# Kernel optimization log

Hardware: AMD Instinct MI355X
Metric: run time of the kernel (lower is better)

## Reference

```python
import jax, jax.numpy as jnp
import numpy as np


def _layer_norm(x, w, b, eps=1e-5):
    mu = jnp.mean(x, axis=-1, keepdims=True)
    var = jnp.mean((x - mu) ** 2, axis=-1, keepdims=True)
    return (x - mu) / jnp.sqrt(var + eps) * w + b


def _s4_block(u, log_dt, A_re, A_im, C_re, C_im, D, out_w, out_b):
    # u: (B, L, H). S4D diagonal SSM, bidirectional, ZOH discretization.
    B, L, H = u.shape
    dt = jnp.exp(log_dt)                       # (H,)
    A = A_re + 1j * A_im                       # (H, N) complex64
    dtA = A * dt[:, None]                      # (H, N)
    C = C_re + 1j * C_im                       # (2, H, N)
    Ct = C * ((jnp.exp(dtA) - 1.0) / A)        # (2, H, N)  ZOH input matrix folded into C
    vand = jnp.exp(dtA[:, :, None] * jnp.arange(L))   # (H, N, L) vandermonde of exp(dt*A)
    K = 2.0 * jnp.einsum('chn,hnl->chl', Ct, vand).real  # (2, H, L); 2*Re for conj pairs
    # bidirectional kernel laid out over length 2L (forward causal + flipped anticausal)
    k = jnp.pad(K[0], ((0, 0), (0, L))) + jnp.pad(jnp.flip(K[1], -1), ((0, 0), (L, 0)))
    k_f = jnp.fft.rfft(k, n=2 * L, axis=-1)    # (H, L+1)
    u_f = jnp.fft.rfft(u, n=2 * L, axis=1)     # (B, L+1, H)
    y = jnp.fft.irfft(u_f * k_f.T[None], n=2 * L, axis=1)[:, :L]  # (B, L, H)
    y = y + u * D                              # skip connection D*u
    y = jax.nn.gelu(y, approximate=False)      # torch GELU is exact erf form
    z = y @ out_w.T + out_b                    # (B, L, 2H) output linear
    return z[..., :H] * jax.nn.sigmoid(z[..., H:])  # GLU


def setup_inputs() -> dict:
    key = jax.random.key(0)
    ks = jax.random.split(key, 10)
    B, L, H, N, NL = 8, 4096, 512, 16, 4
    x = jax.random.normal(ks[0], (B, 1, L), dtype=jnp.float32)
    enc_w = jax.random.normal(ks[1], (H, 2), dtype=jnp.float32) * 0.1
    enc_b = jnp.zeros((H,), jnp.float32)
    # S4D-Lin init: dt log-uniform in [1e-3, 1e-1], A = -0.5 + i*pi*n
    log_dt = np.log(1e-3) + jax.random.uniform(ks[2], (NL, H), dtype=jnp.float32) * (np.log(1e-1) - np.log(1e-3))
    A_re = -0.5 * jnp.ones((NL, H, N), jnp.float32)
    A_im = jnp.broadcast_to(np.pi * jnp.arange(N, dtype=jnp.float32), (NL, H, N))
    C_re = jax.random.normal(ks[3], (NL, 2, H, N), dtype=jnp.float32) * 0.5
    C_im = jax.random.normal(ks[4], (NL, 2, H, N), dtype=jnp.float32) * 0.5
    D = jax.random.normal(ks[5], (NL, H), dtype=jnp.float32)
    out_w = jax.random.normal(ks[6], (NL, 2 * H, H), dtype=jnp.float32) / np.sqrt(H)
    out_b = jnp.zeros((NL, 2 * H), jnp.float32)
    ln_w = jnp.ones((NL, H), jnp.float32)
    ln_b = jnp.zeros((NL, H), jnp.float32)
    dec_w = jax.random.normal(ks[7], (1, H), dtype=jnp.float32) / np.sqrt(H)
    dec_b = jnp.zeros((1,), jnp.float32)
    return dict(x=x, enc_w=enc_w, enc_b=enc_b, log_dt=log_dt, A_re=A_re, A_im=A_im,
                C_re=C_re, C_im=C_im, D=D, out_w=out_w, out_b=out_b,
                ln_w=ln_w, ln_b=ln_b, dec_w=dec_w, dec_b=dec_b)


def reference(x, enc_w, enc_b, log_dt, A_re, A_im, C_re, C_im, D, out_w, out_b, ln_w, ln_b, dec_w, dec_b):
    B, _, L = x.shape
    grid = jnp.linspace(0.0, 1.0, L, dtype=x.dtype)                    # get_grid with grid=None
    h = jnp.concatenate([x.transpose(0, 2, 1),
                         jnp.broadcast_to(grid[None, :, None], (B, L, 1))], axis=-1)  # (B, L, 2)
    h = h @ enc_w.T + enc_b                                            # encoder -> (B, L, H)
    n_layers = log_dt.shape[0]
    for i in range(n_layers):                                          # prenorm residual stack
        z = _layer_norm(h, ln_w[i], ln_b[i])
        z = _s4_block(z, log_dt[i], A_re[i], A_im[i], C_re[i], C_im[i], D[i], out_w[i], out_b[i])
        h = z + h                                                      # dropout is identity (eval)
    y = h @ dec_w.T + dec_b                                            # decoder -> (B, L, 1)
    return y.transpose(0, 2, 1)                                        # (B, 1, L)
```

## Files before the change

kernel.cpp:

```cpp
#include <hip/hip_runtime.h>


typedef __attribute__((ext_vector_type(8))) short s16x8;
typedef __attribute__((ext_vector_type(4))) float f32x4;
typedef unsigned short u16;
typedef unsigned int u32;

#define LSEQ 4096
#define HD   512
#define NST  16
#define NLAYER 4
#define BS   8
#define LC   64
#define NCH  64
#define BC   512

static __device__ __forceinline__ u16 f2bf(float f){
  u32 u = __builtin_bit_cast(u32, f);
  u += 0x7FFFu + ((u >> 16) & 1u);
  return (u16)(u >> 16);
}
static __device__ __forceinline__ float bf2f(u16 v){
  u32 u = ((u32)v) << 16;
  return __builtin_bit_cast(float, u);
}
static __device__ __forceinline__ u32 pack2bf(float a, float b){
  return (u32)f2bf(a) | ((u32)f2bf(b) << 16);
}
static __device__ __forceinline__ float gelu_exact(float x){
  float z = fabsf(x) * 0.70710678118654752f;
  float t = 1.f / (1.f + 0.3275911f * z);
  float p = t*(0.254829592f + t*(-0.284496736f + t*(1.421413741f +
            t*(-1.453152027f + t*1.061405429f))));
  float er = 1.f - p * expf(-z*z);
  er = (x < 0.f) ? -er : er;
  return 0.5f * x * (1.f + er);
}
static __device__ __forceinline__ void async16(const void* g, void* l){
  __builtin_amdgcn_global_load_lds((const __attribute__((address_space(1))) unsigned*)g,
                                   (__attribute__((address_space(3))) unsigned*)l,
                                   16, 0, 0);
}

__global__ __launch_bounds__(256) void param_kernel(
    const float* __restrict__ log_dt, const float* __restrict__ A_re,
    const float* __restrict__ A_im, const float* __restrict__ C_re,
    const float* __restrict__ C_im, float* __restrict__ params)
{
  int idx = blockIdx.x*256 + threadIdx.x;
  int h = idx & (HD-1);
  int n = (idx >> 9) & (NST-1);
  int layer = idx >> 13;
  float dt  = expf(log_dt[layer*HD + h]);
  float Are = A_re[((layer<<9)+h)*NST + n];
  float Aim = A_im[((layer<<9)+h)*NST + n];
  float ar = Are*dt, ai = Aim*dt;
  float er = expf(ar), sn, cs;
  sincosf(ai, &sn, &cs);
  float wr = er*cs, wi = er*sn;
  float eL = expf((float)LC*ar), snL, csL;
  sincosf((float)LC*ai, &snL, &csL);
  float* P = params + layer*65536;
  P[n*1024 + h]        = wr;
  P[n*1024 + 512 + h]  = wi;
  P[16384 + n*1024 + h]       = eL*csL;
  P[16384 + n*1024 + 512 + h] = eL*snL;
  float den = Are*Are + Aim*Aim;
  float qr = ((wr-1.f)*Are + wi*Aim) / den;
  float qi = (wi*Are - (wr-1.f)*Aim) / den;
  #pragma unroll
  for (int d=0; d<2; d++){
    float Cre = C_re[(((layer*2+d)<<9)+h)*NST + n];
    float Cim = C_im[(((layer*2+d)<<9)+h)*NST + n];
    P[32768 + (d*NST+n)*1024 + h]       = 2.f*(Cre*qr - Cim*qi);
    P[32768 + (d*NST+n)*1024 + 512 + h] = 2.f*(Cre*qi + Cim*qr);
  }
}

__global__ __launch_bounds__(256) void owconv_kernel(const float* __restrict__ ow,
                                                     u16* __restrict__ owbf)
{
  size_t idx = (size_t)blockIdx.x*256 + threadIdx.x;
  owbf[idx] = f2bf(ow[idx]);
}

__global__ __launch_bounds__(256) void encoder_kernel(
    const float* __restrict__ x, const float* __restrict__ ew,
    const float* __restrict__ eb, float* __restrict__ hbuf,
    float2* __restrict__ pstat)
{
  int row  = (int)((blockIdx.x*256 + threadIdx.x) >> 6);
  int lane = threadIdx.x & 63;
  int t = row & (LSEQ-1);
  int b = row >> 12;
  float xv = x[(b<<12) + t];
  float g = (float)t * (1.0f/4095.0f);
  const float* ewp = ew + lane*16;
  const float* ebp = eb + lane*8;
  float hv[8], s = 0.f, sq = 0.f;
  #pragma unroll
  for (int j=0;j<8;++j){
    float v = xv*ewp[2*j] + g*ewp[2*j+1] + ebp[j];
    hv[j] = v; s += v; sq += v*v;
  }
  float4* hp = (float4*)(hbuf + ((size_t)row << 9) + lane*8);
  hp[0] = make_float4(hv[0],hv[1],hv[2],hv[3]);
  hp[1] = make_float4(hv[4],hv[5],hv[6],hv[7]);
  #pragma unroll
  for (int off=32; off; off>>=1){ s += __shfl_xor(s, off, 64); sq += __shfl_xor(sq, off, 64); }
  if (lane < 8) pstat[(size_t)row*8 + lane] = (lane==0) ? make_float2(s, sq)
                                                        : make_float2(0.f, 0.f);
}

__global__ __launch_bounds__(256) void lnt_kernel(
    const float* __restrict__ hbuf, const float2* __restrict__ pstat,
    const float* __restrict__ lnw, const float* __restrict__ lnb,
    u16* __restrict__ uT)
{
  __shared__ u32 tile[512*33];
  __shared__ float smu[64], srs[64];
  int bc = blockIdx.x, tid = threadIdx.x;
  const float* base = hbuf + ((size_t)bc << 15);
  if (tid < 64){
    const float2* pp = pstat + ((size_t)(bc*64 + tid))*8;
    float s = 0.f, sq = 0.f;
    #pragma unroll
    for (int j=0;j<8;++j){ float2 v = pp[j]; s += v.x; sq += v.y; }
    float mu = s*(1.f/512.f);
    float var = sq*(1.f/512.f) - mu*mu;
    smu[tid] = mu; srs[tid] = rsqrtf(var + 1e-5f);
  }
  __syncthreads();
  #pragma unroll
  for (int it=0; it<8; ++it){
    int ho = (tid & 7) + it*8;
    int tp = (tid >> 3) & 31;
    int r0 = 2*tp, r1 = 2*tp + 1;
    float mu0 = smu[r0], rs0 = srs[r0];
    float mu1 = smu[r1], rs1 = srs[r1];
    const float* pa = base + ((size_t)r0 << 9) + ho*8;
    const float* pc = base + ((size_t)r1 << 9) + ho*8;
    float4 a0 = *(const float4*)pa, a1 = *(const float4*)(pa+4);
    float4 c0 = *(const float4*)pc, c1 = *(const float4*)(pc+4);
    const float* pw = lnw + ho*8;
    const float* pb = lnb + ho*8;
    float4 w0 = *(const float4*)pw, w1 = *(const float4*)(pw+4);
    float4 b0 = *(const float4*)pb, b1 = *(const float4*)(pb+4);
    u32* td = &tile[(ho*8)*33 + tp];
    td[0*33] = pack2bf((a0.x-mu0)*rs0*w0.x+b0.x, (c0.x-mu1)*rs1*w0.x+b0.x);
    td[1*33] = pack2bf((a0.y-mu0)*rs0*w0.y+b0.y, (c0.y-mu1)*rs1*w0.y+b0.y);
    td[2*33] = pack2bf((a0.z-mu0)*rs0*w0.z+b0.z, (c0.z-mu1)*rs1*w0.z+b0.z);
    td[3*33] = pack2bf((a0.w-mu0)*rs0*w0.w+b0.w, (c0.w-mu1)*rs1*w0.w+b0.w);
    td[4*33] = pack2bf((a1.x-mu0)*rs0*w1.x+b1.x, (c1.x-mu1)*rs1*w1.x+b1.x);
    td[5*33] = pack2bf((a1.y-mu0)*rs0*w1.y+b1.y, (c1.y-mu1)*rs1*w1.y+b1.y);
    td[6*33] = pack2bf((a1.z-mu0)*rs0*w1.z+b1.z, (c1.z-mu1)*rs1*w1.z+b1.z);
    td[7*33] = pack2bf((a1.w-mu0)*rs0*w1.w+b1.w, (c1.w-mu1)*rs1*w1.w+b1.w);
  }
  __syncthreads();
  #pragma unroll
  for (int it=0; it<16; ++it){
    int linear = it*256 + tid;
    int h = linear >> 3, sg = linear & 7;
    uint4 v = *(const uint4*)&tile[h*33 + sg*4];
    *(uint4*)(uT + ((size_t)h*BC + bc)*64 + sg*8) = v;
  }
}

__global__ __launch_bounds__(256) void build_kernel(
    const float* __restrict__ logdt, const float* __restrict__ Are_,
    const float* __restrict__ Aim_, const float* __restrict__ P,
    const float* __restrict__ Dv, u16* __restrict__ Abuf, u16* __restrict__ Wbuf)
{
  __shared__ float pr[65][17], pi[65][17];
  __shared__ float kp0[4][64], kp1[4][64];
  __shared__ float kk0[64], kk1[64];
  int h = blockIdx.x;
  int tid = threadIdx.x;
  int d = tid & 63, ng = tid >> 6;
  float dt = expf(logdt[h]);
  float k0p = 0.f, k1p = 0.f;
  #pragma unroll
  for (int j=0; j<4; ++j){
    int n = ng*4 + j;
    float ar = Are_[h*NST+n]*dt, ai = Aim_[h*NST+n]*dt;
    float er = expf(ar*(float)d), sn, cs;
    sincosf(ai*(float)d, &sn, &cs);
    float wr = er*cs, wi = er*sn;
    pr[d][n] = wr; pi[d][n] = wi;
    if (d == 63){
      float er2 = expf(ar*64.f), sn2, cs2;
      sincosf(ai*64.f, &sn2, &cs2);
      pr[64][n] = er2*cs2; pi[64][n] = er2*sn2;
    }
    float c0r = P[32768 + n*1024 + h],      c0i = P[32768 + n*1024 + 512 + h];
    float c1r = P[32768 + (16+n)*1024 + h], c1i = P[32768 + (16+n)*1024 + 512 + h];
    k0p += c0r*wr - c0i*wi;
    k1p += c1r*wr - c1i*wi;
  }
  kp0[ng][d] = k0p; kp1[ng][d] = k1p;
  __syncthreads();
  if (ng == 0){
    kk0[d] = kp0[0][d]+kp0[1][d]+kp0[2][d]+kp0[3][d];
    kk1[d] = kp1[0][d]+kp1[1][d]+kp1[2][d]+kp1[3][d];
  }
  __syncthreads();
  {
    int r = d;
    u32* wdst = (u32*)(Wbuf + (size_t)h*4096 + r*64);
    int n = r & 15;
    #pragma unroll
    for (int k=0;k<8;++k){
      int s2 = ng*8 + k;
      int s0 = 2*s2, s1 = s0+1;
      float va, vb;
      if      (r < 16){ va = pr[63-s0][n]; vb = pr[63-s1][n]; }
      else if (r < 32){ va = pi[63-s0][n]; vb = pi[63-s1][n]; }
      else if (r < 48){ va = pr[s0][n];    vb = pr[s1][n]; }
      else            { va = pi[s0][n];    vb = pi[s1][n]; }
      wdst[s2] = pack2bf(va, vb);
    }
  }
  {
    int t = d;
    float Dh = Dv[h];
    u32* adst = (u32*)(Abuf + (size_t)h*8192 + t*128);
    #pragma unroll
    for (int k=0;k<8;++k){
      int j2 = ng*8 + k;
      int j0 = 2*j2, j1 = j0+1;
      float va = (j0 < t) ? kk0[t-j0] : ((j0 == t) ? (kk0[0] + Dh) : kk1[j0-t-1]);
      float vb = (j1 < t) ? kk0[t-j1] : ((j1 == t) ? (kk0[0] + Dh) : kk1[j1-t-1]);
      adst[j2] = pack2bf(va, vb);
    }
    #pragma unroll
    for (int j=0;j<4;j+=2){
      int n = ng*4 + j;
      float ar0 = pr[t+1][n],   ai0 = pi[t+1][n];
      float ar1 = pr[t+1][n+1], ai1 = pi[t+1][n+1];
      float br0 = pr[63-t][n],   bi0 = pi[63-t][n];
      float br1 = pr[63-t][n+1], bi1 = pi[63-t][n+1];
      float c0r0 = P[32768 + n*1024 + h],     c0i0 = P[32768 + n*1024 + 512 + h];
      float c0r1 = P[32768 + (n+1)*1024 + h], c0i1 = P[32768 + (n+1)*1024 + 512 + h];
      float c1r0 = P[32768 + (16+n)*1024 + h], c1i0 = P[32768 + (16+n)*1024 + 512 + h];
      float c1r1 = P[32768 + (17+n)*1024 + h], c1i1 = P[32768 + (17+n)*1024 + 512 + h];
      int g = n >> 1;
      adst[32      + g] = pack2bf(c0r0*ar0 - c0i0*ai0,    c0r1*ar1 - c0i1*ai1);
      adst[32 + 8  + g] = pack2bf(-(c0r0*ai0 + c0i0*ar0), -(c0r1*ai1 + c0i1*ar1));
      adst[32 + 16 + g] = pack2bf(c1r0*br0 - c1i0*bi0,    c1r1*br1 - c1i1*bi1);
      adst[32 + 24 + g] = pack2bf(-(c1r0*bi0 + c1i0*br0), -(c1r1*bi1 + c1i1*br1));
    }
  }
}

__global__ __launch_bounds__(256) void ssm_kernel(
    const float* __restrict__ P, const u16* __restrict__ Wbuf,
    const u16* __restrict__ Abuf, const u16* __restrict__ uT,
    u16* __restrict__ yT)
{
  __shared__ u16 Ul[256*64];
  __shared__ u16 Vl[256*64];
  const int h = blockIdx.x;
  const int tid = threadIdx.x;
  const int wave = tid >> 6, lane = tid & 63;
  const int ro = lane & 15, qq = lane >> 4;
  const int sx = ro & 7;
  const u16* Wh = Wbuf + (size_t)h*4096;
  const u16* Ah = Abuf + (size_t)h*8192;
  const u16* Uh = uT + (size_t)h*BC*64;

  for (int half=0; half<2; ++half){
    if (half) __syncthreads();
    #pragma unroll
    for (int i=0; i<8; ++i){
      int r = i*32 + (tid >> 3);
      int gch = tid & 7;
      const u16* src = Uh + ((size_t)(half*256 + r))*64 + ((gch ^ (r & 7)) << 3);
      async16(src, &Ul[i*2048 + tid*8]);
    }
    __syncthreads();
    {
      f32x4 acc[4][4];
      #pragma unroll
      for (int i=0;i<4;i++)
        #pragma unroll
        for (int j=0;j<4;j++)
          #pragma unroll
          for (int k=0;k<4;k++) acc[i][j][k] = 0.f;
      #pragma unroll
      for (int ks=0; ks<2; ++ks){
        int g = ks*4 + qq;
        s16x8 a[4], b[4];
        #pragma unroll
        for (int mt=0; mt<4; ++mt){
          uint4 v = *(const uint4*)(Wh + (mt*16 + ro)*64 + ks*32 + qq*8);
          a[mt] = __builtin_bit_cast(s16x8, v);
        }
        #pragma unroll
        for (int nt=0; nt<4; ++nt){
          int bl = wave*64 + nt*16 + ro;
          uint4 v = *(const uint4*)(&Ul[bl*64 + ((g ^ sx) << 3)]);
          b[nt] = __builtin_bit_cast(s16x8, v);
        }
        #pragma unroll
        for (int mt=0; mt<4; ++mt)
          #pragma unroll
          for (int nt=0; nt<4; ++nt)
            acc[mt][nt] = __builtin_amdgcn_mfma_f32_16x16x32_bf16(a[mt], b[nt], acc[mt][nt], 0, 0, 0);
      }
      #pragma unroll
      for (int mt=0; mt<4; ++mt)
        #pragma unroll
        for (int nt=0; nt<4; ++nt){
          int bl = wave*64 + nt*16 + ro;
          int r0 = mt*16 + qq*4;
          u32 lo = pack2bf(acc[mt][nt][0], acc[mt][nt][1]);
          u32 hi = pack2bf(acc[mt][nt][2], acc[mt][nt][3]);
          int addr = bl*64 + (((r0 >> 3) ^ (bl & 7)) << 3) + (r0 & 7);
          *(uint2*)(&Vl[addr]) = make_uint2(lo, hi);
        }
    }
    __syncthreads();
    if (tid < 128){
      int n   = tid & 15;
      int bl4 = (tid >> 4) & 3;
      int dir = (tid >> 6) & 1;
      float wLr = P[16384 + n*1024 + h];
      float wLi = P[16384 + n*1024 + 512 + h];
      float Xr = 0.f, Xi = 0.f;
      if (dir == 0){
        int kA = n, kB = 16 + n;
        for (int c=0; c<NCH; ++c){
          int bl = bl4*64 + c;
          int aA = bl*64 + (((kA >> 3) ^ (c & 7)) << 3) + (kA & 7);
          int aB = bl*64 + (((kB >> 3) ^ (c & 7)) << 3) + (kB & 7);
          float sr = bf2f(Vl[aA]), si = bf2f(Vl[aB]);
          Vl[aA] = f2bf(Xr); Vl[aB] = f2bf(Xi);
          float nr = fmaf(wLr, Xr, fmaf(-wLi, Xi, sr));
          float ni = fmaf(wLr, Xi, fmaf( wLi, Xr, si));
          Xr = nr; Xi = ni;
        }
      } else {
        int kA = 32 + n, kB = 48 + n;
        for (int cc=0; cc<NCH; ++cc){
          int c = NCH-1-cc;
          int bl = bl4*64 + c;
          int aA = bl*64 + (((kA >> 3) ^ (c & 7)) << 3) + (kA & 7);
          int aB = bl*64 + (((kB >> 3) ^ (c & 7)) << 3) + (kB & 7);
          float sr = bf2f(Vl[aA]), si = bf2f(Vl[aB]);
          Vl[aA] = f2bf(Xr); Vl[aB] = f2bf(Xi);
          float nr = fmaf(wLr, Xr, fmaf(-wLi, Xi, sr));
          float ni = fmaf(wLr, Xi, fmaf( wLi, Xr, si));
          Xr = nr; Xi = ni;
        }
      }
    }
    __syncthreads();
    {
      f32x4 acc[4][4];
      #pragma unroll
      for (int i=0;i<4;i++)
        #pragma unroll
        for (int j=0;j<4;j++)
          #pragma unroll
          for (int k=0;k<4;k++) acc[i][j][k] = 0.f;
      #pragma unroll
      for (int ks=0; ks<4; ++ks){
        const u16* Bsrc = (ks < 2) ? Ul : Vl;
        int g = (ks & 1)*4 + qq;
        s16x8 a[4], b[4];
        #pragma unroll
        for (int mt=0; mt<4; ++mt){
          uint4 v = *(const uint4*)(Ah + (mt*16 + ro)*128 + ks*32 + qq*8);
          a[mt] = __builtin_bit_cast(s16x8, v);
        }
        #pragma unroll
        for (int nt=0; nt<4; ++nt){
          int bl = wave*64 + nt*16 + ro;
          uint4 v = *(const uint4*)(&Bsrc[bl*64 + ((g ^ sx) << 3)]);
          b[nt] = __builtin_bit_cast(s16x8, v);
        }
        #pragma unroll
        for (int mt=0; mt<4; ++mt)
          #pragma unroll
          for (int nt=0; nt<4; ++nt)
            acc[mt][nt] = __builtin_amdgcn_mfma_f32_16x16x32_bf16(a[mt], b[nt], acc[mt][nt], 0, 0, 0);
      }
      #pragma unroll
      for (int mt=0; mt<4; ++mt)
        #pragma unroll
        for (int nt=0; nt<4; ++nt){
          int bc = half*256 + wave*64 + nt*16 + ro;
          int t0 = mt*16 + qq*4;
          u32 lo = pack2bf(gelu_exact(acc[mt][nt][0]), gelu_exact(acc[mt][nt][1]));
          u32 hi = pack2bf(gelu_exact(acc[mt][nt][2]), gelu_exact(acc[mt][nt][3]));
          *(uint2*)(yT + ((size_t)h*BC + bc)*64 + t0) = make_uint2(lo, hi);
        }
    }
  }
}

__global__ __launch_bounds__(256) void t2_kernel(const u16* __restrict__ yT,
                                                 u16* __restrict__ uy)
{
  __shared__ u32 tile[64*257];
  int bc = blockIdx.x, tid = threadIdx.x;
  #pragma unroll
  for (int it=0; it<8; ++it){
    int sg = tid & 7;
    int hp = it*32 + (tid >> 3);
    const u16* s0 = yT + ((size_t)(2*hp)*BC + bc)*64 + sg*8;
    uint4 a = *(const uint4*)s0;
    uint4 b = *(const uint4*)(s0 + (size_t)BC*64);
    u32 ua[4] = {a.x,a.y,a.z,a.w}, ub[4] = {b.x,b.y,b.z,b.w};
    #pragma unroll
    for (int w=0; w<4; ++w){
      u32 lo = (ua[w] & 0xFFFFu) | (ub[w] << 16);
      u32 hi = (ua[w] >> 16) | (ub[w] & 0xFFFF0000u);
      tile[(sg*8 + 2*w    )*257 + hp] = lo;
      tile[(sg*8 + 2*w + 1)*257 + hp] = hi;
    }
  }
  __syncthreads();
  #pragma unroll
  for (int it=0; it<16; ++it){
    int linear = it*256 + tid;
    int t = linear >> 6, sg = linear & 63;
    uint4 v = *(const uint4*)&tile[t*257 + sg*4];
    *(uint4*)(uy + ((size_t)(bc*64 + t) << 9) + sg*8) = v;
  }
}

__global__ __launch_bounds__(256) void gemm_glu_kernel(
    const u16* __restrict__ ybf, const u16* __restrict__ owbf,
    const float* __restrict__ ob, float* __restrict__ hbuf,
    float2* __restrict__ pstat)
{
  __shared__ u16 As[128*64];
  __shared__ u16 Bsh[128*64];
  const int tid = threadIdx.x;
  const int wave = tid >> 6, lane = tid & 63;
  const int x7 = blockIdx.x & 7;
  const int nt = (blockIdx.x >> 3) & 7;
  const int mt = (blockIdx.x >> 6)*8 + x7;
  const int m0 = mt*128, n0 = nt*64;
  const int row = tid >> 3;
  const int ch  = tid & 7;
  f32x4 acc[2][8];
  #pragma unroll
  for (int i=0;i<2;i++)
    #pragma unroll
    for (int j=0;j<8;j++)
      #pragma unroll
      for (int k=0;k<4;k++) acc[i][j][k] = 0.f;

  const int ro = lane & 15, qq = lane >> 4;
  const int sx = ro & 7;
  for (int k0=0;k0<512;k0+=64){
    __syncthreads();
    #pragma unroll
    for (int p=0;p<4;p++){
      int r = p*32 + row;
      int cs = (ch ^ (r & 7)) << 3;
      async16(ybf + ((size_t)(m0+r) << 9) + k0 + cs, &As[(r<<6) + (ch<<3)]);
      int br = n0 + (r & 63) + ((r >> 6) << 9);
      async16(owbf + ((size_t)br << 9) + k0 + cs, &Bsh[(r<<6) + (ch<<3)]);
    }
    __syncthreads();
    #pragma unroll
    for (int ks=0;ks<2;ks++){
      s16x8 a[2], bf[8];
      #pragma unroll
      for (int mi=0;mi<2;mi++){
        int g = ks*4 + qq;
        uint4 t = *(const uint4*)(&As[((wave*32 + mi*16 + ro)<<6) + ((g ^ sx)<<3)]);
        a[mi] = __builtin_bit_cast(s16x8, t);
      }
      #pragma unroll
      for (int ni=0;ni<8;ni++){
        int g = ks*4 + qq;
        uint4 t = *(const uint4*)(&Bsh[((ni*16 + ro)<<6) + ((g ^ sx)<<3)]);
        bf[ni] = __builtin_bit_cast(s16x8, t);
      }
      #pragma unroll
      for (int mi=0;mi<2;mi++)
        #pragma unroll
        for (int ni=0;ni<8;ni++)
          acc[mi][ni] = __builtin_amdgcn_mfma_f32_16x16x32_bf16(a[mi], bf[ni], acc[mi][ni], 0, 0, 0);
    }
  }
  float b1v[4], b2v[4];
  #pragma unroll
  for (int ni=0;ni<4;ni++){ b1v[ni] = ob[n0 + ni*16 + ro]; b2v[ni] = ob[n0 + ni*16 + ro + 512]; }
  #pragma unroll
  for (int mi=0;mi<2;mi++){
    #pragma unroll
    for (int rg=0;rg<4;rg++){
      int rowi = m0 + wave*32 + mi*16 + qq*4 + rg;
      float s = 0.f, sq = 0.f;
      #pragma unroll
      for (int ni=0;ni<4;ni++){
        int col = n0 + ni*16 + ro;
        float zz1 = acc[mi][ni][rg] + b1v[ni];
        float zz2 = acc[mi][ni+4][rg] + b2v[ni];
        float g = zz1 / (1.f + expf(-zz2));
        size_t idx = ((size_t)rowi << 9) + col;
        float hn = hbuf[idx] + g;
        hbuf[idx] = hn;
        s += hn; sq += hn*hn;
      }
      #pragma unroll
      for (int off=1; off<16; off<<=1){ s += __shfl_xor(s, off, 64); sq += __shfl_xor(sq, off, 64); }
      if (ro == 0) pstat[(size_t)rowi*8 + nt] = make_float2(s, sq);
    }
  }
}

__global__ __launch_bounds__(256) void decoder_kernel(
    const float* __restrict__ hbuf, const float* __restrict__ dec_w,
    const float* __restrict__ dec_b, float* __restrict__ out)
{
  int wid  = (int)((blockIdx.x*256 + threadIdx.x) >> 6);
  int lane = threadIdx.x & 63;
  const float* p = hbuf + ((size_t)wid << 9) + lane*8;
  float4 a = *(const float4*)p;
  float4 b = *(const float4*)(p+4);
  const float* dw = dec_w + lane*8;
  float4 w0 = *(const float4*)dw;
  float4 w1 = *(const float4*)(dw+4);
  float s = a.x*w0.x + a.y*w0.y + a.z*w0.z + a.w*w0.w
          + b.x*w1.x + b.y*w1.y + b.z*w1.z + b.w*w1.w;
  #pragma unroll
  for (int off=32; off; off>>=1) s += __shfl_xor(s, off, 64);
  if (lane == 0) out[wid] = s + dec_b[0];
}

extern "C" void kernel_launch(void* const* d_in, const int* in_sizes, int n_in,
                              void* d_out, int out_size, void* d_ws, size_t ws_size,
                              hipStream_t stream) {
  const float* x     = (const float*)d_in[0];
  const float* encw  = (const float*)d_in[1];
  const float* encb  = (const float*)d_in[2];
  const float* logdt = (const float*)d_in[3];
  const float* A_re  = (const float*)d_in[4];
  const float* A_im  = (const float*)d_in[5];
  const float* C_re  = (const float*)d_in[6];
  const float* C_im  = (const float*)d_in[7];
  const float* Dv    = (const float*)d_in[8];
  const float* out_w = (const float*)d_in[9];
  const float* out_b = (const float*)d_in[10];
  const float* ln_w  = (const float*)d_in[11];
  const float* ln_b  = (const float*)d_in[12];
  const float* dec_w = (const float*)d_in[13];
  const float* dec_b = (const float*)d_in[14];

  char* ws = (char*)d_ws;
  float*  hbuf   = (float*) (ws);
  u16*    uy     = (u16*)   (ws + 67108864);
  u16*    uT     = (u16*)   (ws + 100663296);
  u16*    yT     = (u16*)   (ws + 134217728);
  u16*    owbf   = (u16*)   (ws + 201326592);
  float*  params = (float*) (ws + 205520896);
  u16*    Abuf   = (u16*)   (ws + 206569472);
  u16*    Wbuf   = (u16*)   (ws + 214958080);
  float2* pstat  = (float2*)(ws + 219152384);

  param_kernel<<<128, 256, 0, stream>>>(logdt, A_re, A_im, C_re, C_im, params);
  owconv_kernel<<<8192, 256, 0, stream>>>(out_w, owbf);
  encoder_kernel<<<8192, 256, 0, stream>>>(x, encw, encb, hbuf, pstat);
  for (int layer=0; layer<NLAYER; ++layer){
    const float* P = params + layer*65536;
    lnt_kernel<<<512, 256, 0, stream>>>(hbuf, pstat, ln_w + layer*HD, ln_b + layer*HD, uT);
    build_kernel<<<512, 256, 0, stream>>>(logdt + layer*HD, A_re + layer*HD*NST,
                                          A_im + layer*HD*NST, P, Dv + layer*HD,
                                          Abuf, Wbuf);
    ssm_kernel<<<512, 256, 0, stream>>>(P, Wbuf, Abuf, uT, yT);
    t2_kernel<<<512, 256, 0, stream>>>(yT, uy);
    gemm_glu_kernel<<<2048, 256, 0, stream>>>(uy, owbf + (size_t)layer*524288,
                                              out_b + layer*1024, hbuf, pstat);
  }
  decoder_kernel<<<8192, 256, 0, stream>>>(hbuf, dec_w, dec_b, (float*)d_out);
}
```

Baseline: 764.1 us.

## Split SSM kernel across four blocks per channel and use fast exp intrinsics

```diff
diff --git a/kernel.cpp b/kernel.cpp
--- a/kernel.cpp
+++ b/kernel.cpp
@@ -32,7 +32,7 @@
   float t = 1.f / (1.f + 0.3275911f * z);
   float p = t*(0.254829592f + t*(-0.284496736f + t*(1.421413741f +
             t*(-1.453152027f + t*1.061405429f))));
-  float er = 1.f - p * expf(-z*z);
+  float er = 1.f - p * __expf(-z*z);
   er = (x < 0.f) ? -er : er;
   return 0.5f * x * (1.f + er);
 }
@@ -257,9 +257,10 @@
     const u16* __restrict__ Abuf, const u16* __restrict__ uT,
     u16* __restrict__ yT)
 {
-  __shared__ u16 Ul[256*64];
-  __shared__ u16 Vl[256*64];
-  const int h = blockIdx.x;
+  __shared__ u16 Ul[128*64];
+  __shared__ u16 Vl[128*64];
+  const int h = blockIdx.x >> 2;
+  const int q = blockIdx.x & 3;
   const int tid = threadIdx.x;
   const int wave = tid >> 6, lane = tid & 63;
   const int ro = lane & 15, qq = lane >> 4;
@@ -268,134 +269,132 @@
   const u16* Ah = Abuf + (size_t)h*8192;
   const u16* Uh = uT + (size_t)h*BC*64;
 
-  for (int half=0; half<2; ++half){
-    if (half) __syncthreads();
-    #pragma unroll
-    for (int i=0; i<8; ++i){
-      int r = i*32 + (tid >> 3);
-      int gch = tid & 7;
-      const u16* src = Uh + ((size_t)(half*256 + r))*64 + ((gch ^ (r & 7)) << 3);
-      async16(src, &Ul[i*2048 + tid*8]);
-    }
-    __syncthreads();
-    {
-      f32x4 acc[4][4];
-      #pragma unroll
-      for (int i=0;i<4;i++)
+  #pragma unroll
+  for (int i=0; i<4; ++i){
+    int r = i*32 + (tid >> 3);
+    int gch = tid & 7;
+    const u16* src = Uh + ((size_t)(q*128 + r))*64 + ((gch ^ (r & 7)) << 3);
+    async16(src, &Ul[i*2048 + tid*8]);
+  }
+  __syncthreads();
+  {
+    f32x4 acc[4][2];
+    #pragma unroll
+    for (int i=0;i<4;i++)
+      #pragma unroll
+      for (int j=0;j<2;j++)
         #pragma unroll
-        for (int j=0;j<4;j++)
-          #pragma unroll
-          for (int k=0;k<4;k++) acc[i][j][k] = 0.f;
-      #pragma unroll
-      for (int ks=0; ks<2; ++ks){
-        int g = ks*4 + qq;
-        s16x8 a[4], b[4];
-        #pragma unroll
-        for (int mt=0; mt<4; ++mt){
-          uint4 v = *(const uint4*)(Wh + (mt*16 + ro)*64 + ks*32 + qq*8);
-          a[mt] = __builtin_bit_cast(s16x8, v);
-        }
-        #pragma unroll
-        for (int nt=0; nt<4; ++nt){
-          int bl = wave*64 + nt*16 + ro;
-          uint4 v = *(const uint4*)(&Ul[bl*64 + ((g ^ sx) << 3)]);
-          b[nt] = __builtin_bit_cast(s16x8, v);
-        }
-        #pragma unroll
-        for (int mt=0; mt<4; ++mt)
-          #pragma unroll
-          for (int nt=0; nt<4; ++nt)
-            acc[mt][nt] = __builtin_amdgcn_mfma_f32_16x16x32_bf16(a[mt], b[nt], acc[mt][nt], 0, 0, 0);
+        for (int k=0;k<4;k++) acc[i][j][k] = 0.f;
+    #pragma unroll
+    for (int ks=0; ks<2; ++ks){
+      int g = ks*4 + qq;
+      s16x8 a[4], b[2];
+      #pragma unroll
+      for (int mt=0; mt<4; ++mt){
+        uint4 v = *(const uint4*)(Wh + (mt*16 + ro)*64 + ks*32 + qq*8);
+        a[mt] = __builtin_bit_cast(s16x8, v);
+      }
+      #pragma unroll
+      for (int nt=0; nt<2; ++nt){
+        int bl = wave*32 + nt*16 + ro;
+        uint4 v = *(const uint4*)(&Ul[bl*64 + ((g ^ sx) << 3)]);
+        b[nt] = __builtin_bit_cast(s16x8, v);
       }
       #pragma unroll
       for (int mt=0; mt<4; ++mt)
         #pragma unroll
-        for (int nt=0; nt<4; ++nt){
-          int bl = wave*64 + nt*16 + ro;
-          int r0 = mt*16 + qq*4;
-          u32 lo = pack2bf(acc[mt][nt][0], acc[mt][nt][1]);
-          u32 hi = pack2bf(acc[mt][nt][2], acc[mt][nt][3]);
-          int addr = bl*64 + (((r0 >> 3) ^ (bl & 7)) << 3) + (r0 & 7);
-          *(uint2*)(&Vl[addr]) = make_uint2(lo, hi);
-        }
-    }
-    __syncthreads();
-    if (tid < 128){
-      int n   = tid & 15;
-      int bl4 = (tid >> 4) & 3;
-      int dir = (tid >> 6) & 1;
-      float wLr = P[16384 + n*1024 + h];
-      float wLi = P[16384 + n*1024 + 512 + h];
-      float Xr = 0.f, Xi = 0.f;
-      if (dir == 0){
-        int kA = n, kB = 16 + n;
-        for (int c=0; c<NCH; ++c){
-          int bl = bl4*64 + c;
-          int aA = bl*64 + (((kA >> 3) ^ (c & 7)) << 3) + (kA & 7);
-          int aB = bl*64 + (((kB >> 3) ^ (c & 7)) << 3) + (kB & 7);
-          float sr = bf2f(Vl[aA]), si = bf2f(Vl[aB]);
-          Vl[aA] = f2bf(Xr); Vl[aB] = f2bf(Xi);
-          float nr = fmaf(wLr, Xr, fmaf(-wLi, Xi, sr));
-          float ni = fmaf(wLr, Xi, fmaf( wLi, Xr, si));
-          Xr = nr; Xi = ni;
-        }
-      } else {
-        int kA = 32 + n, kB = 48 + n;
-        for (int cc=0; cc<NCH; ++cc){
-          int c = NCH-1-cc;
-          int bl = bl4*64 + c;
-          int aA = bl*64 + (((kA >> 3) ^ (c & 7)) << 3) + (kA & 7);
-          int aB = bl*64 + (((kB >> 3) ^ (c & 7)) << 3) + (kB & 7);
-          float sr = bf2f(Vl[aA]), si = bf2f(Vl[aB]);
-          Vl[aA] = f2bf(Xr); Vl[aB] = f2bf(Xi);
-          float nr = fmaf(wLr, Xr, fmaf(-wLi, Xi, sr));
-          float ni = fmaf(wLr, Xi, fmaf( wLi, Xr, si));
-          Xr = nr; Xi = ni;
-        }
-      }
-    }
-    __syncthreads();
-    {
-      f32x4 acc[4][4];
-      #pragma unroll
-      for (int i=0;i<4;i++)
+        for (int nt=0; nt<2; ++nt)
+          acc[mt][nt] = __builtin_amdgcn_mfma_f32_16x16x32_bf16(a[mt], b[nt], acc[mt][nt], 0, 0, 0);
+    }
+    #pragma unroll
+    for (int mt=0; mt<4; ++mt)
+      #pragma unroll
+      for (int nt=0; nt<2; ++nt){
+        int bl = wave*32 + nt*16 + ro;
+        int r0 = mt*16 + qq*4;
+        u32 lo = pack2bf(acc[mt][nt][0], acc[mt][nt][1]);
+        u32 hi = pack2bf(acc[mt][nt][2], acc[mt][nt][3]);
+        int addr = bl*64 + (((r0 >> 3) ^ (bl & 7)) << 3) + (r0 & 7);
+        *(uint2*)(&Vl[addr]) = make_uint2(lo, hi);
+      }
+  }
+  __syncthreads();
+  if (tid < 128 && (tid & 63) < 32){
+    int ln  = tid & 63;
+    int dir = tid >> 6;
+    int n   = ln & 15;
+    int b2  = ln >> 4;
+    float wLr = P[16384 + n*1024 + h];
+    float wLi = P[16384 + n*1024 + 512 + h];
+    float Xr = 0.f, Xi = 0.f;
+    if (dir == 0){
+      int kA = n, kB = 16 + n;
+      for (int c=0; c<NCH; ++c){
+        int bl = b2*64 + c;
+        int aA = bl*64 + (((kA >> 3) ^ (bl & 7)) << 3) + (kA & 7);
+        int aB = bl*64 + (((kB >> 3) ^ (bl & 7)) << 3) + (kB & 7);
+        float sr = bf2f(Vl[aA]), si = bf2f(Vl[aB]);
+        Vl[aA] = f2bf(Xr); Vl[aB] = f2bf(Xi);
+        float nr = fmaf(wLr, Xr, fmaf(-wLi, Xi, sr));
+        float ni = fmaf(wLr, Xi, fmaf( wLi, Xr, si));
+        Xr = nr; Xi = ni;
+      }
+    } else {
+      int kA = 32 + n, kB = 48 + n;
+      for (int cc=0; cc<NCH; ++cc){
+        int c = NCH-1-cc;
+        int bl = b2*64 + c;
+        int aA = bl*64 + (((kA >> 3) ^ (bl & 7)) << 3) + (kA & 7);
+        int aB = bl*64 + (((kB >> 3) ^ (bl & 7)) << 3) + (kB & 7);
+        float sr = bf2f(Vl[aA]), si = bf2f(Vl[aB]);
+        Vl[aA] = f2bf(Xr); Vl[aB] = f2bf(Xi);
+        float nr = fmaf(wLr, Xr, fmaf(-wLi, Xi, sr));
+        float ni = fmaf(wLr, Xi, fmaf( wLi, Xr, si));
+        Xr = nr; Xi = ni;
+      }
+    }
+  }
+  __syncthreads();
+  {
+    f32x4 acc[4][2];
+    #pragma unroll
+    for (int i=0;i<4;i++)
+      #pragma unroll
+      for (int j=0;j<2;j++)
         #pragma unroll
-        for (int j=0;j<4;j++)
-          #pragma unroll
-          for (int k=0;k<4;k++) acc[i][j][k] = 0.f;
-      #pragma unroll
-      for (int ks=0; ks<4; ++ks){
-        const u16* Bsrc = (ks < 2) ? Ul : Vl;
-        int g = (ks & 1)*4 + qq;
-        s16x8 a[4], b[4];
-        #pragma unroll
-        for (int mt=0; mt<4; ++mt){
-          uint4 v = *(const uint4*)(Ah + (mt*16 + ro)*128 + ks*32 + qq*8);
-          a[mt] = __builtin_bit_cast(s16x8, v);
-        }
-        #pragma unroll
-        for (int nt=0; nt<4; ++nt){
-          int bl = wave*64 + nt*16 + ro;
-          uint4 v = *(const uint4*)(&Bsrc[bl*64 + ((g ^ sx) << 3)]);
-          b[nt] = __builtin_bit_cast(s16x8, v);
-        }
-        #pragma unroll
-        for (int mt=0; mt<4; ++mt)
-          #pragma unroll
-          for (int nt=0; nt<4; ++nt)
-            acc[mt][nt] = __builtin_amdgcn_mfma_f32_16x16x32_bf16(a[mt], b[nt], acc[mt][nt], 0, 0, 0);
+        for (int k=0;k<4;k++) acc[i][j][k] = 0.f;
+    #pragma unroll
+    for (int ks=0; ks<4; ++ks){
+      const u16* Bsrc = (ks < 2) ? Ul : Vl;
+      int g = (ks & 1)*4 + qq;
+      s16x8 a[4], b[2];
+      #pragma unroll
+      for (int mt=0; mt<4; ++mt){
+        uint4 v = *(const uint4*)(Ah + (mt*16 + ro)*128 + ks*32 + qq*8);
+        a[mt] = __builtin_bit_cast(s16x8, v);
+      }
+      #pragma unroll
+      for (int nt=0; nt<2; ++nt){
+        int bl = wave*32 + nt*16 + ro;
+        uint4 v = *(const uint4*)(&Bsrc[bl*64 + ((g ^ sx) << 3)]);
+        b[nt] = __builtin_bit_cast(s16x8, v);
       }
       #pragma unroll
       for (int mt=0; mt<4; ++mt)
         #pragma unroll
-        for (int nt=0; nt<4; ++nt){
-          int bc = half*256 + wave*64 + nt*16 + ro;
-          int t0 = mt*16 + qq*4;
-          u32 lo = pack2bf(gelu_exact(acc[mt][nt][0]), gelu_exact(acc[mt][nt][1]));
-          u32 hi = pack2bf(gelu_exact(acc[mt][nt][2]), gelu_exact(acc[mt][nt][3]));
-          *(uint2*)(yT + ((size_t)h*BC + bc)*64 + t0) = make_uint2(lo, hi);
-        }
-    }
+        for (int nt=0; nt<2; ++nt)
+          acc[mt][nt] = __builtin_amdgcn_mfma_f32_16x16x32_bf16(a[mt], b[nt], acc[mt][nt], 0, 0, 0);
+    }
+    #pragma unroll
+    for (int mt=0; mt<4; ++mt)
+      #pragma unroll
+      for (int nt=0; nt<2; ++nt){
+        int bc = q*128 + wave*32 + nt*16 + ro;
+        int t0 = mt*16 + qq*4;
+        u32 lo = pack2bf(gelu_exact(acc[mt][nt][0]), gelu_exact(acc[mt][nt][1]));
+        u32 hi = pack2bf(gelu_exact(acc[mt][nt][2]), gelu_exact(acc[mt][nt][3]));
+        *(uint2*)(yT + ((size_t)h*BC + bc)*64 + t0) = make_uint2(lo, hi);
+      }
   }
 }
 
@@ -502,7 +501,7 @@
         int col = n0 + ni*16 + ro;
         float zz1 = acc[mi][ni][rg] + b1v[ni];
         float zz2 = acc[mi][ni+4][rg] + b2v[ni];
-        float g = zz1 / (1.f + expf(-zz2));
+        float g = __fdividef(zz1, 1.f + __expf(-zz2));
         size_t idx = ((size_t)rowi << 9) + col;
         float hn = hbuf[idx] + g;
         hbuf[idx] = hn;
@@ -573,7 +572,7 @@
     build_kernel<<<512, 256, 0, stream>>>(logdt + layer*HD, A_re + layer*HD*NST,
                                           A_im + layer*HD*NST, P, Dv + layer*HD,
                                           Abuf, Wbuf);
-    ssm_kernel<<<512, 256, 0, stream>>>(P, Wbuf, Abuf, uT, yT);
+    ssm_kernel<<<2048, 256, 0, stream>>>(P, Wbuf, Abuf, uT, yT);
     t2_kernel<<<512, 256, 0, stream>>>(yT, uy);
     gemm_glu_kernel<<<2048, 256, 0, stream>>>(uy, owbf + (size_t)layer*524288,
                                               out_b + layer*1024, hbuf, pstat);
```

After: 701.0 us. 8.3% less time.
